# Optimization experiments

Hardware: AMD Instinct MI355X
Metric: run time of the kernel (lower is better)

## Reference

```python
import jax, jax.numpy as jnp
import numpy as np

MAX_DIST = 20
N_HEADS = 8
LN_EPS = 1e-5


def _layer_norm(x, g, b):
    mu = jnp.mean(x, axis=-1, keepdims=True)
    var = jnp.var(x, axis=-1, keepdims=True)
    return (x - mu) / jnp.sqrt(var + LN_EPS) * g + b


def setup_inputs() -> dict:
    key = jax.random.key(0)
    ks = jax.random.split(key, 12)
    B, N, D, H, F = 8, 1024, 768, N_HEADS, 1024
    w = lambda k, *sh: (jax.random.normal(k, sh, jnp.float32) * 0.02)
    return {
        "x": jax.random.normal(ks[0], (B, N, D), jnp.float32),
        "node_mask": jnp.ones((B, N), jnp.int32),
        "centers": jnp.arange(B * N, dtype=jnp.float32).reshape(B, N),
        "types": jax.random.randint(ks[1], (B, N), 0, 2, jnp.int32),
        # params (torch Linear weights stored transposed as [in, out])
        "qkv_w": w(ks[2], D, 3 * D), "qkv_b": jnp.zeros((3 * D,), jnp.float32),
        "out_w": w(ks[3], D, D), "out_b": jnp.zeros((D,), jnp.float32),
        "ff1_w": w(ks[4], D, F), "ff1_b": jnp.zeros((F,), jnp.float32),
        "ff2_w": w(ks[5], F, D), "ff2_b": jnp.zeros((D,), jnp.float32),
        "ln1_g": jnp.ones((D,), jnp.float32), "ln1_b": jnp.zeros((D,), jnp.float32),
        "ln2_g": jnp.ones((D,), jnp.float32), "ln2_b": jnp.zeros((D,), jnp.float32),
        "rel_emb": w(ks[6], 2 * MAX_DIST + 1, H),  # relative-distance bias table
        "tt": w(ks[7], H, 2, 2),                   # type-pair bias table
    }


def reference(x, node_mask, centers, types,
              qkv_w, qkv_b, out_w, out_b,
              ff1_w, ff1_b, ff2_w, ff2_b,
              ln1_g, ln1_b, ln2_g, ln2_b,
              rel_emb, tt):
    B, N, D = x.shape
    H = rel_emb.shape[1]
    Dh = D // H

    qkv = x @ qkv_w + qkv_b                       # [B,N,3D]
    q, k, v = jnp.split(qkv, 3, axis=-1)
    split = lambda t: t.reshape(B, N, H, Dh).transpose(0, 2, 1, 3)  # [B,H,N,Dh]
    q, k, v = split(q), split(k), split(v)

    scores = jnp.einsum("bhid,bhjd->bhij", q, k) / np.sqrt(Dh).astype(np.float32)

    # relative-position bias: bucket clamped distance into [0, 2*max_dist]
    dist = centers[:, :, None] - centers[:, None, :]              # [B,N,N]
    idx = jnp.round(jnp.clip(dist, -MAX_DIST, MAX_DIST) + MAX_DIST).astype(jnp.int32)
    rb = rel_emb[idx].transpose(0, 3, 1, 2)                       # [B,H,N,N]

    # type-pair bias
    ti = jnp.broadcast_to(types[:, :, None], (B, N, N))
    tj = jnp.broadcast_to(types[:, None, :], (B, N, N))
    tb = tt[:, ti, tj].transpose(1, 0, 2, 3)                      # [B,H,N,N]

    scores = scores + rb + tb
    mask = node_mask[:, None, None, :]                            # [B,1,1,N]
    scores = jnp.where(mask == 0, -jnp.inf, scores)
    att = jax.nn.softmax(scores, axis=-1)
    att = jnp.nan_to_num(att, nan=0.0)

    y = jnp.einsum("bhij,bhjd->bhid", att, v)
    y = y.transpose(0, 2, 1, 3).reshape(B, N, D)
    y = y @ out_w + out_b

    x = _layer_norm(x + y, ln1_g, ln1_b)
    ff = jax.nn.gelu(x @ ff1_w + ff1_b, approximate=False) @ ff2_w + ff2_b
    x = _layer_norm(x + ff, ln2_g, ln2_b)
    return x
```

## Files before the change

kernel.cpp:

```cpp
#include <hip/hip_runtime.h>

typedef short short8 __attribute__((ext_vector_type(8)));
typedef unsigned short ushort8v __attribute__((ext_vector_type(8)));
typedef float f32x4 __attribute__((ext_vector_type(4)));

static __device__ __forceinline__ unsigned short f2b(float f) {
    unsigned int u = __builtin_bit_cast(unsigned int, f);
    unsigned int r = (u + 0x7fffu + ((u >> 16) & 1u)) >> 16;
    return (unsigned short)r;
}
static __device__ __forceinline__ unsigned short f2b_trunc(float f) {
    return (unsigned short)(__builtin_bit_cast(unsigned int, f) >> 16);
}
static __device__ __forceinline__ float b2f(unsigned short u) {
    return __builtin_bit_cast(float, (unsigned int)u << 16);
}
static __device__ __forceinline__ float exp2v(float x) {
    float r;
    asm("v_exp_f32 %0, %1" : "=v"(r) : "v"(x));
    return r;
}

__device__ __forceinline__ void gload16(void* lds, const void* g) {
    __builtin_amdgcn_global_load_lds(
        (const __attribute__((address_space(1))) void*)g,
        (__attribute__((address_space(3))) void*)lds, 16, 0, 0);
}

#define L2E 1.4426950408889634f

__global__ __launch_bounds__(256) void prep_kernel(
    const float* __restrict__ x, unsigned short* __restrict__ xb,
    const float* __restrict__ qkv_w, unsigned short* __restrict__ qwT,
    const float* __restrict__ out_w, unsigned short* __restrict__ owT,
    const float* __restrict__ ff1_w, unsigned short* __restrict__ f1T,
    const float* __restrict__ ff2_w, unsigned short* __restrict__ f2T) {
    const int bx = blockIdx.x;
    const int tid = threadIdx.x;
    if (bx < 6144) {
        int i = bx * 256 + tid;
        float4 f = ((const float4*)x)[i];
        ushort4 u;
        u.x = f2b(f.x); u.y = f2b(f.y); u.z = f2b(f.z); u.w = f2b(f.w);
        ((ushort4*)xb)[i] = u;
        return;
    }
    __shared__ float t[32][33];
    int rb = bx - 6144;
    const float* W; unsigned short* Wt; int K, N;
    if (rb < 1728)      { W = qkv_w; Wt = qwT; K = 768;  N = 2304; }
    else if (rb < 2304) { rb -= 1728; W = out_w; Wt = owT; K = 768;  N = 768; }
    else if (rb < 3072) { rb -= 2304; W = ff1_w; Wt = f1T; K = 768;  N = 1024; }
    else                { rb -= 3072; W = ff2_w; Wt = f2T; K = 1024; N = 768; }
    const int nbl = N / 32;
    const int nb = (rb % nbl) * 32, kb = (rb / nbl) * 32;
    const int tx = tid & 31, ty = tid >> 5;
#pragma unroll
    for (int i = 0; i < 32; i += 8)
        t[ty + i][tx] = W[(size_t)(kb + ty + i) * N + nb + tx];
    __syncthreads();
#pragma unroll
    for (int i = 0; i < 32; i += 8)
        Wt[(size_t)(nb + ty + i) * K + kb + tx] = f2b(t[tx][ty + i]);
}

template <int EPI>
__global__ __launch_bounds__(512, 4) void gemm2p(
    const unsigned short* __restrict__ A, const unsigned short* __restrict__ Bt,
    const float* __restrict__ bias, float* __restrict__ outf,
    unsigned short* __restrict__ outb, unsigned short* __restrict__ q_o,
    unsigned short* __restrict__ k_o, unsigned short* __restrict__ v_o,
    int N, int K, int ntn, int NT) {
    __shared__ unsigned short a_lds[2][8192];
    __shared__ unsigned short b_lds[2][8192];
    const int tid = threadIdx.x;
    const int wave = tid >> 6, lane = tid & 63;
    const int lr = lane & 15, lg = lane >> 4;
    const int wm = wave >> 2, wn = wave & 3;
    const int nwg = gridDim.x;
    const int orig = blockIdx.x;
    const int swz = (orig & 7) * (nwg >> 3) + (orig >> 3);
    const int tm = swz / ntn, tn = swz % ntn;

    const unsigned short* srcA[2];
    const unsigned short* srcB[2];
#pragma unroll
    for (int i = 0; i < 2; ++i) {
        int g = i * 512 + tid;
        int row = g >> 3, sl = g & 7;
        int colg = sl ^ (row & 7);
        srcA[i] = A + (size_t)(tm * 128 + row) * K + colg * 8;
        srcB[i] = Bt + (size_t)(tn * 128 + row) * K + colg * 8;
    }
    auto stage = [&](int buf, int k0) {
#pragma unroll
        for (int i = 0; i < 2; ++i) {
            gload16(&a_lds[buf][i * 4096 + wave * 512], srcA[i] + k0);
            gload16(&b_lds[buf][i * 4096 + wave * 512], srcB[i] + k0);
        }
    };

    f32x4 acc[4][2] = {};

    stage(0, 0);
    asm volatile("s_waitcnt vmcnt(0)" ::: "memory");
    __builtin_amdgcn_s_barrier();

    for (int t = 0; t < NT; ++t) {
        const int buf = t & 1;
        if (t + 1 < NT) stage(buf ^ 1, (t + 1) * 64);
#pragma unroll
        for (int ks = 0; ks < 2; ++ks) {
            short8 af[4], bfr[2];
#pragma unroll
            for (int mf = 0; mf < 4; ++mf) {
                int row = wm * 64 + mf * 16 + lr;
                int slot = (ks * 4 + lg) ^ (row & 7);
                af[mf] = *(const short8*)&a_lds[buf][row * 64 + slot * 8];
            }
#pragma unroll
            for (int nf = 0; nf < 2; ++nf) {
                int row = wn * 32 + nf * 16 + lr;
                int slot = (ks * 4 + lg) ^ (row & 7);
                bfr[nf] = *(const short8*)&b_lds[buf][row * 64 + slot * 8];
            }
#pragma unroll
            for (int mf = 0; mf < 4; ++mf)
#pragma unroll
                for (int nf = 0; nf < 2; ++nf)
                    acc[mf][nf] = __builtin_amdgcn_mfma_f32_16x16x32_bf16(af[mf], bfr[nf], acc[mf][nf], 0, 0, 0);
        }
        asm volatile("s_waitcnt vmcnt(0)" ::: "memory");
        __builtin_amdgcn_s_barrier();
    }

#pragma unroll
    for (int nf = 0; nf < 2; ++nf) {
        int gc = tn * 128 + wn * 32 + nf * 16 + lr;
        float bv = bias[gc];
        int part = 0, h = 0, dh = 0;
        if constexpr (EPI == 3) {
            part = gc / 768;
            int cc = gc - part * 768;
            h = cc / 96;
            dh = cc - h * 96;
        }
#pragma unroll
        for (int mf = 0; mf < 4; ++mf) {
            int grb = tm * 128 + wm * 64 + mf * 16 + lg * 4;
            if constexpr (EPI == 3) {
                int b = grb >> 10, n2 = grb & 1023;
                size_t bh = (size_t)(b * 8 + h);
                if (part == 2) {
                    ushort4 wv;
                    wv.x = f2b(acc[mf][nf][0] + bv);
                    wv.y = f2b(acc[mf][nf][1] + bv);
                    wv.z = f2b(acc[mf][nf][2] + bv);
                    wv.w = f2b(acc[mf][nf][3] + bv);
                    *(ushort4*)&v_o[(bh * 96 + dh) * 1024 + n2] = wv;
                } else {
                    unsigned short* dst = (part == 0) ? q_o : k_o;
                    float sc = (part == 0) ? 0.14724445f : 1.f;
#pragma unroll
                    for (int r = 0; r < 4; ++r)
                        dst[(bh * 1024 + n2 + r) * 96 + dh] = f2b((acc[mf][nf][r] + bv) * sc);
                }
            } else {
#pragma unroll
                for (int r = 0; r < 4; ++r) {
                    int gr = grb + r;
                    float v = acc[mf][nf][r] + bv;
                    if constexpr (EPI == 0) {
                        outf[(size_t)gr * N + gc] = v;
                    } else if constexpr (EPI == 1) {
                        outb[(size_t)gr * N + gc] = f2b(v);
                    } else {
                        float gl = 0.5f * v * (1.f + erff(v * 0.70710678f));
                        outb[(size_t)gr * N + gc] = f2b(gl);
                    }
                }
            }
        }
    }
}

__global__ __launch_bounds__(512, 4) void attn_kernel(
    const unsigned short* __restrict__ Qb, const unsigned short* __restrict__ Kb,
    const unsigned short* __restrict__ Vt, const float* __restrict__ centers,
    const int* __restrict__ types, const int* __restrict__ nmask,
    const float* __restrict__ tt, const float* __restrict__ rel_emb,
    unsigned short* __restrict__ Y) {
    __shared__ unsigned short kv_lds[2 * 12288];
    __shared__ unsigned short p_lds[8 * 1024];
    __shared__ float c_lds[1024];
    __shared__ unsigned int bab_lds[1024];
    __shared__ float rel_lds[41];

    const int tid = threadIdx.x;
    const int wave = tid >> 6, lane = tid & 63;
    const int lr = lane & 15, lg = lane >> 4;
    const int bh = blockIdx.x, qb = blockIdx.y;
    const int b = bh >> 3, h = bh & 7;
    const int q0 = qb * 128 + wave * 16;
    const size_t kvbase = (size_t)bh * 1024 * 96;

    c_lds[tid] = centers[b * 1024 + tid];
    c_lds[tid + 512] = centers[b * 1024 + 512 + tid];
    if (tid < 41) rel_lds[tid] = rel_emb[tid * 8 + h] * L2E;
    {
        const float t00 = tt[h * 4], t01 = tt[h * 4 + 1];
        const float t10 = tt[h * 4 + 2], t11 = tt[h * 4 + 3];
#pragma unroll
        for (int i = 0; i < 2; ++i) {
            int j = tid + i * 512;
            int tj = types[b * 1024 + j];
            int mk = nmask[b * 1024 + j];
            float bA = L2E * (t00 + (t01 - t00) * tj) + (mk ? 0.f : -1e30f);
            float bB = L2E * ((t10 - t00) + (t11 - t01 - t10 + t00) * tj);
            bab_lds[j] = (unsigned)f2b(bA) | ((unsigned)f2b(bB) << 16);
        }
    }

    const unsigned short* sbase[3];
    int sstep[3];
#pragma unroll
    for (int it = 0; it < 3; ++it) {
        int g = it * 512 + tid;
        if (g < 768) {
            int ks = g >> 8, rem = g & 255, pr = rem >> 3, sl = rem & 7;
            int so = sl ^ (pr & 7);
            int r = ((so >> 2) << 5) + pr, oct = so & 3;
            sbase[it] = Kb + kvbase + (size_t)r * 96 + ks * 32 + oct * 8;
            sstep[it] = 64 * 96;
        } else {
            int gv = g - 768, pr = gv >> 3, sl = gv & 7;
            int so = sl ^ (pr & 7);
            sbase[it] = Vt + (size_t)(bh * 96 + pr) * 1024 + so * 8;
            sstep[it] = 64;
        }
    }
    auto stage = [&](int bufb, int kt) {
        unsigned short* dst = kv_lds + bufb * 12288;
#pragma unroll
        for (int it = 0; it < 3; ++it)
            gload16(dst + it * 4096 + wave * 512, sbase[it] + (size_t)kt * sstep[it]);
    };

    short8 qa[3];
#pragma unroll
    for (int ks = 0; ks < 3; ++ks)
        qa[ks] = *(const short8*)&Qb[kvbase + (size_t)(q0 + lr) * 96 + ks * 32 + lg * 8];
    short8 qa3 = {};
    {
        int ti0 = types[b * 1024 + q0 + lr];
        if (lg == 0) {
            qa3[0] = (short)0x3F80;
            qa3[1] = ti0 ? (short)0x3F80 : (short)0;
        }
    }
    float ci20[4];
#pragma unroll
    for (int r = 0; r < 4; ++r) ci20[r] = centers[b * 1024 + q0 + lg * 4 + r] + 20.f;

    float cimax20 = fmaxf(fmaxf(ci20[0], ci20[1]), fmaxf(ci20[2], ci20[3]));
    float cimin20 = fminf(fminf(ci20[0], ci20[1]), fminf(ci20[2], ci20[3]));
    cimax20 = fmaxf(cimax20, __shfl_xor(cimax20, 16));
    cimax20 = fmaxf(cimax20, __shfl_xor(cimax20, 32));
    cimin20 = fminf(cimin20, __shfl_xor(cimin20, 16));
    cimin20 = fminf(cimin20, __shfl_xor(cimin20, 32));

    short8 vone = {};
    if (lr == 0) {
#pragma unroll
        for (int e = 0; e < 8; ++e) vone[e] = (short)0x3F80;
    }

    float m_r[4] = {-3e30f, -3e30f, -3e30f, -3e30f};
    f32x4 oacc[7] = {};

    stage(0, 0);
    asm volatile("s_waitcnt lgkmcnt(0)" ::: "memory");
    const float rel0v = rel_lds[0], rel40v = rel_lds[40];

    for (int kt = 0; kt < 16; ++kt) {
        const int buf = kt & 1;
        if (kt < 15) {
            stage(buf ^ 1, kt + 1);
            asm volatile("s_waitcnt vmcnt(3)" ::: "memory");
        } else {
            asm volatile("s_waitcnt vmcnt(0)" ::: "memory");
        }
        __builtin_amdgcn_s_barrier();
        const unsigned short* kv = kv_lds + buf * 12288;

        f32x4 s[4] = {};
#pragma unroll
        for (int jf = 0; jf < 4; ++jf) {
            int pr = ((jf & 1) << 4) + lr;
            int slp = (((jf >> 1) << 2) + lg) ^ (lr & 7);
#pragma unroll
            for (int ks = 0; ks < 3; ++ks) {
                short8 kf = *(const short8*)&kv[ks * 2048 + pr * 64 + slp * 8];
                s[jf] = __builtin_amdgcn_mfma_f32_16x16x32_bf16(qa[ks], kf, s[jf], 0, 0, 0);
            }
            unsigned vb = bab_lds[kt * 64 + jf * 16 + lr];
            short8 kf3 = {};
            if (lg == 0) {
                kf3[0] = (short)(vb & 0xffffu);
                kf3[1] = (short)(vb >> 16);
            }
            s[jf] = __builtin_amdgcn_mfma_f32_16x16x32_bf16(qa3, kf3, s[jf], 0, 0, 0);
        }

        {
            float cj[4];
#pragma unroll
            for (int jf = 0; jf < 4; ++jf) cj[jf] = c_lds[kt * 64 + jf * 16 + lr];
            float cjmx = fmaxf(fmaxf(cj[0], cj[1]), fmaxf(cj[2], cj[3]));
            float cjmn = fminf(fminf(cj[0], cj[1]), fminf(cj[2], cj[3]));
#pragma unroll
            for (int off = 1; off < 16; off <<= 1) {
                cjmx = fmaxf(cjmx, __shfl_xor(cjmx, off));
                cjmn = fminf(cjmn, __shfl_xor(cjmn, off));
            }
            bool flatHi = (cimin20 - cjmx >= 40.f);
            bool flatLo = (cimax20 - cjmn <= 0.f);
            if (flatHi || flatLo) {
                float re = flatHi ? rel40v : rel0v;
#pragma unroll
                for (int jf = 0; jf < 4; ++jf)
#pragma unroll
                    for (int r = 0; r < 4; ++r) s[jf][r] += re;
            } else {
#pragma unroll
                for (int jf = 0; jf < 4; ++jf)
#pragma unroll
                    for (int r = 0; r < 4; ++r) {
                        float idxf = __builtin_amdgcn_fmed3f(ci20[r] - cj[jf], 0.f, 40.f);
                        s[jf][r] += rel_lds[(int)rintf(idxf)];
                    }
            }
        }

#pragma unroll
        for (int r = 0; r < 4; ++r) {
            float mlr = fmaxf(fmaxf(s[0][r], s[1][r]), fmaxf(s[2][r], s[3][r]));
            if (!__all(mlr <= m_r[r] + 8.f)) {
                float mx = mlr;
#pragma unroll
                for (int off = 1; off < 16; off <<= 1) mx = fmaxf(mx, __shfl_xor(mx, off));
                float mn = fmaxf(m_r[r], mx);
                float al = exp2v(m_r[r] - mn);
                m_r[r] = mn;
#pragma unroll
                for (int nf = 0; nf < 7; ++nf) oacc[nf][r] *= al;
            }
#pragma unroll
            for (int jf = 0; jf < 4; ++jf) s[jf][r] = exp2v(s[jf][r] - m_r[r]);
        }

#pragma unroll
        for (int jf = 0; jf < 4; ++jf)
#pragma unroll
            for (int r = 0; r < 4; ++r) {
                int row = lg * 4 + r, col = jf * 16 + lr;
                int gp = (col >> 3) ^ (row & 7);
                p_lds[wave * 1024 + row * 64 + gp * 8 + (col & 7)] = f2b_trunc(s[jf][r]);
            }
        asm volatile("s_waitcnt lgkmcnt(0)" ::: "memory");
        short8 pa[2];
#pragma unroll
        for (int js = 0; js < 2; ++js) {
            int slp = ((js << 2) + lg) ^ (lr & 7);
            pa[js] = *(const short8*)&p_lds[wave * 1024 + lr * 64 + slp * 8];
        }

#pragma unroll
        for (int nf = 0; nf < 6; ++nf) {
            int vrow = nf * 16 + lr;
#pragma unroll
            for (int js = 0; js < 2; ++js) {
                int slp = ((js << 2) + lg) ^ (lr & 7);
                short8 vf = *(const short8*)&kv[6144 + vrow * 64 + slp * 8];
                oacc[nf] = __builtin_amdgcn_mfma_f32_16x16x32_bf16(pa[js], vf, oacc[nf], 0, 0, 0);
            }
        }
#pragma unroll
        for (int js = 0; js < 2; ++js)
            oacc[6] = __builtin_amdgcn_mfma_f32_16x16x32_bf16(pa[js], vone, oacc[6], 0, 0, 0);
        __builtin_amdgcn_s_barrier();
    }

#pragma unroll
    for (int r = 0; r < 4; ++r) {
        float l = __shfl(oacc[6][r], lane & 48);
        float inv = (l > 0.f) ? 1.f / l : 0.f;
        int qi = q0 + lg * 4 + r;
#pragma unroll
        for (int nf = 0; nf < 6; ++nf)
            Y[((size_t)b * 1024 + qi) * 768 + h * 96 + nf * 16 + lr] = f2b(oacc[nf][r] * inv);
    }
}

template <bool IN1BF, bool IN2BF>
__global__ __launch_bounds__(384) void ln_kernel(const void* __restrict__ in1,
                                                 const void* __restrict__ in2,
                                                 const float* __restrict__ g,
                                                 const float* __restrict__ be,
                                                 float* __restrict__ of,
                                                 unsigned short* __restrict__ ob) {
    const int tid = threadIdx.x;
    const int half = tid / 192;
    const int t = tid - half * 192;
    const int row = blockIdx.x * 2 + half;
    const size_t base = (size_t)row * 768 + t * 4;
    float a[4], bb[4];
    if (IN1BF) {
        ushort4 u = *(const ushort4*)((const unsigned short*)in1 + base);
        a[0] = b2f(u.x); a[1] = b2f(u.y); a[2] = b2f(u.z); a[3] = b2f(u.w);
    } else {
        float4 u = *(const float4*)((const float*)in1 + base);
        a[0] = u.x; a[1] = u.y; a[2] = u.z; a[3] = u.w;
    }
    if (IN2BF) {
        ushort4 u = *(const ushort4*)((const unsigned short*)in2 + base);
        bb[0] = b2f(u.x); bb[1] = b2f(u.y); bb[2] = b2f(u.z); bb[3] = b2f(u.w);
    } else {
        float4 u = *(const float4*)((const float*)in2 + base);
        bb[0] = u.x; bb[1] = u.y; bb[2] = u.z; bb[3] = u.w;
    }
    float v[4];
#pragma unroll
    for (int i = 0; i < 4; ++i) v[i] = a[i] + bb[i];
    float s1 = v[0] + v[1] + v[2] + v[3];
    float s2 = v[0] * v[0] + v[1] * v[1] + v[2] * v[2] + v[3] * v[3];
#pragma unroll
    for (int off = 32; off > 0; off >>= 1) {
        s1 += __shfl_xor(s1, off);
        s2 += __shfl_xor(s2, off);
    }
    __shared__ float red[12];
    const int wv = tid >> 6;
    if ((tid & 63) == 0) { red[wv] = s1; red[6 + wv] = s2; }
    __syncthreads();
    const int w0 = half * 3;
    s1 = red[w0] + red[w0 + 1] + red[w0 + 2];
    s2 = red[6 + w0] + red[6 + w0 + 1] + red[6 + w0 + 2];
    float mu = s1 * (1.f / 768.f);
    float var = s2 * (1.f / 768.f) - mu * mu;
    float inv = rsqrtf(var + 1e-5f);
    float o[4];
#pragma unroll
    for (int i = 0; i < 4; ++i)
        o[i] = (v[i] - mu) * inv * g[t * 4 + i] + be[t * 4 + i];
    if (of) {
        float4 w = {o[0], o[1], o[2], o[3]};
        *(float4*)(of + base) = w;
    }
    if (ob) {
        ushort4 w = {f2b(o[0]), f2b(o[1]), f2b(o[2]), f2b(o[3])};
        *(ushort4*)(ob + base) = w;
    }
}

extern "C" void kernel_launch(void* const* d_in, const int* in_sizes, int n_in,
                              void* d_out, int out_size, void* d_ws, size_t ws_size,
                              hipStream_t stream) {
    const float* x     = (const float*)d_in[0];
    const int*   nmask = (const int*)d_in[1];
    const float* cent  = (const float*)d_in[2];
    const int*   types = (const int*)d_in[3];
    const float* qkv_w = (const float*)d_in[4];
    const float* qkv_b = (const float*)d_in[5];
    const float* out_w = (const float*)d_in[6];
    const float* out_b = (const float*)d_in[7];
    const float* ff1_w = (const float*)d_in[8];
    const float* ff1_b = (const float*)d_in[9];
    const float* ff2_w = (const float*)d_in[10];
    const float* ff2_b = (const float*)d_in[11];
    const float* ln1_g = (const float*)d_in[12];
    const float* ln1_b = (const float*)d_in[13];
    const float* ln2_g = (const float*)d_in[14];
    const float* ln2_b = (const float*)d_in[15];
    const float* rel   = (const float*)d_in[16];
    const float* ttp   = (const float*)d_in[17];

    char* w = (char*)d_ws;
    auto alloc = [&](size_t bytes) {
        char* p = w;
        w += (bytes + 255) & ~(size_t)255;
        return p;
    };
    unsigned short* xb  = (unsigned short*)alloc(8192ull * 768 * 2);
    unsigned short* qwT = (unsigned short*)alloc(2304ull * 768 * 2);
    unsigned short* owT = (unsigned short*)alloc(768ull * 768 * 2);
    unsigned short* f1T = (unsigned short*)alloc(1024ull * 768 * 2);
    unsigned short* f2T = (unsigned short*)alloc(768ull * 1024 * 2);
    unsigned short* Qb  = (unsigned short*)alloc(64ull * 1024 * 96 * 2);
    unsigned short* Kb  = (unsigned short*)alloc(64ull * 1024 * 96 * 2);
    unsigned short* Vt  = (unsigned short*)alloc(64ull * 96 * 1024 * 2);
    unsigned short* aob = (unsigned short*)alloc(8192ull * 768 * 2);
    unsigned short* h1b = (unsigned short*)alloc(8192ull * 768 * 2);
    unsigned short* ffa = Qb;

    prep_kernel<<<9984, 256, 0, stream>>>(x, xb, qkv_w, qwT, out_w, owT,
                                          ff1_w, f1T, ff2_w, f2T);

    gemm2p<3><<<1152, 512, 0, stream>>>(xb, qwT, qkv_b, nullptr, nullptr,
                                        Qb, Kb, Vt, 2304, 768, 18, 12);
    attn_kernel<<<dim3(64, 8), 512, 0, stream>>>(Qb, Kb, Vt, cent, types, nmask, ttp, rel, xb);
    gemm2p<1><<<384, 512, 0, stream>>>(xb, owT, out_b, nullptr, aob,
                                       nullptr, nullptr, nullptr, 768, 768, 6, 12);
    ln_kernel<false, true><<<4096, 384, 0, stream>>>(x, aob, ln1_g, ln1_b, nullptr, h1b);
    gemm2p<2><<<512, 512, 0, stream>>>(h1b, f1T, ff1_b, nullptr, ffa,
                                       nullptr, nullptr, nullptr, 1024, 768, 8, 12);
    gemm2p<1><<<384, 512, 0, stream>>>(ffa, f2T, ff2_b, nullptr, aob,
                                       nullptr, nullptr, nullptr, 768, 1024, 6, 16);
    ln_kernel<true, true><<<4096, 384, 0, stream>>>(h1b, aob, ln2_g, ln2_b, (float*)d_out, nullptr);
}
```

Measured before the change: 197.1 us.

## Transpose QK^T MFMA output so softmax rows live per lane

Swaps the MFMA operand order so each lane holds one query row's scores across columns. The softmax max and sum then need only cross-lane-group shuffles, the row sum is accumulated in registers instead of through an extra ones-vector MFMA, and P is written to LDS as packed bf16 pairs with v_cvt_pk_bf16. The rescale factor now has to be shuffled back into the output-accumulator layout, and the P-to-LDS write uses a new swizzle that must match the read pattern. P also changes from truncated to rounded bf16 conversion.

```diff
diff --git a/kernel.cpp b/kernel.cpp
--- a/kernel.cpp
+++ b/kernel.cpp
@@ -9,15 +9,17 @@
     unsigned int r = (u + 0x7fffu + ((u >> 16) & 1u)) >> 16;
     return (unsigned short)r;
 }
-static __device__ __forceinline__ unsigned short f2b_trunc(float f) {
-    return (unsigned short)(__builtin_bit_cast(unsigned int, f) >> 16);
-}
 static __device__ __forceinline__ float b2f(unsigned short u) {
     return __builtin_bit_cast(float, (unsigned int)u << 16);
 }
 static __device__ __forceinline__ float exp2v(float x) {
     float r;
     asm("v_exp_f32 %0, %1" : "=v"(r) : "v"(x));
+    return r;
+}
+static __device__ __forceinline__ unsigned cvt_pk_bf16(float lo, float hi) {
+    unsigned r;
+    asm("v_cvt_pk_bf16_f32 %0, %1, %2" : "=v"(r) : "v"(lo), "v"(hi));
     return r;
 }
 
@@ -258,25 +260,17 @@
             qa3[1] = ti0 ? (short)0x3F80 : (short)0;
         }
     }
-    float ci20[4];
-#pragma unroll
-    for (int r = 0; r < 4; ++r) ci20[r] = centers[b * 1024 + q0 + lg * 4 + r] + 20.f;
-
-    float cimax20 = fmaxf(fmaxf(ci20[0], ci20[1]), fmaxf(ci20[2], ci20[3]));
-    float cimin20 = fminf(fminf(ci20[0], ci20[1]), fminf(ci20[2], ci20[3]));
-    cimax20 = fmaxf(cimax20, __shfl_xor(cimax20, 16));
-    cimax20 = fmaxf(cimax20, __shfl_xor(cimax20, 32));
-    cimin20 = fminf(cimin20, __shfl_xor(cimin20, 16));
-    cimin20 = fminf(cimin20, __shfl_xor(cimin20, 32));
-
-    short8 vone = {};
-    if (lr == 0) {
-#pragma unroll
-        for (int e = 0; e < 8; ++e) vone[e] = (short)0x3F80;
-    }
-
-    float m_r[4] = {-3e30f, -3e30f, -3e30f, -3e30f};
-    f32x4 oacc[7] = {};
+    const float ci20 = centers[b * 1024 + q0 + lr] + 20.f;
+    float cimax20 = ci20, cimin20 = ci20;
+#pragma unroll
+    for (int off = 1; off < 16; off <<= 1) {
+        cimax20 = fmaxf(cimax20, __shfl_xor(cimax20, off));
+        cimin20 = fminf(cimin20, __shfl_xor(cimin20, off));
+    }
+
+    float m_s = -3e30f, l_s = 0.f;
+    f32x4 oacc[6] = {};
+    unsigned* p32 = (unsigned*)&p_lds[wave * 1024];
 
     stage(0, 0);
     asm volatile("s_waitcnt lgkmcnt(0)" ::: "memory");
@@ -301,7 +295,7 @@
 #pragma unroll
             for (int ks = 0; ks < 3; ++ks) {
                 short8 kf = *(const short8*)&kv[ks * 2048 + pr * 64 + slp * 8];
-                s[jf] = __builtin_amdgcn_mfma_f32_16x16x32_bf16(qa[ks], kf, s[jf], 0, 0, 0);
+                s[jf] = __builtin_amdgcn_mfma_f32_16x16x32_bf16(kf, qa[ks], s[jf], 0, 0, 0);
             }
             unsigned vb = bab_lds[kt * 64 + jf * 16 + lr];
             short8 kf3 = {};
@@ -309,20 +303,24 @@
                 kf3[0] = (short)(vb & 0xffffu);
                 kf3[1] = (short)(vb >> 16);
             }
-            s[jf] = __builtin_amdgcn_mfma_f32_16x16x32_bf16(qa3, kf3, s[jf], 0, 0, 0);
+            s[jf] = __builtin_amdgcn_mfma_f32_16x16x32_bf16(kf3, qa3, s[jf], 0, 0, 0);
         }
 
         {
-            float cj[4];
-#pragma unroll
-            for (int jf = 0; jf < 4; ++jf) cj[jf] = c_lds[kt * 64 + jf * 16 + lr];
-            float cjmx = fmaxf(fmaxf(cj[0], cj[1]), fmaxf(cj[2], cj[3]));
-            float cjmn = fminf(fminf(cj[0], cj[1]), fminf(cj[2], cj[3]));
-#pragma unroll
-            for (int off = 1; off < 16; off <<= 1) {
-                cjmx = fmaxf(cjmx, __shfl_xor(cjmx, off));
-                cjmn = fminf(cjmn, __shfl_xor(cjmn, off));
-            }
+            float4 cj4[4];
+#pragma unroll
+            for (int jf = 0; jf < 4; ++jf)
+                cj4[jf] = *(const float4*)&c_lds[kt * 64 + jf * 16 + lg * 4];
+            float cjmx = cj4[0].x, cjmn = cj4[0].x;
+#pragma unroll
+            for (int jf = 0; jf < 4; ++jf) {
+                cjmx = fmaxf(cjmx, fmaxf(fmaxf(cj4[jf].x, cj4[jf].y), fmaxf(cj4[jf].z, cj4[jf].w)));
+                cjmn = fminf(cjmn, fminf(fminf(cj4[jf].x, cj4[jf].y), fminf(cj4[jf].z, cj4[jf].w)));
+            }
+            cjmx = fmaxf(cjmx, __shfl_xor(cjmx, 16));
+            cjmx = fmaxf(cjmx, __shfl_xor(cjmx, 32));
+            cjmn = fminf(cjmn, __shfl_xor(cjmn, 16));
+            cjmn = fminf(cjmn, __shfl_xor(cjmn, 32));
             bool flatHi = (cimin20 - cjmx >= 40.f);
             bool flatLo = (cimax20 - cjmn <= 0.f);
             if (flatHi || flatLo) {
@@ -332,47 +330,67 @@
 #pragma unroll
                     for (int r = 0; r < 4; ++r) s[jf][r] += re;
             } else {
+                float cjl[4][4] = {{cj4[0].x, cj4[0].y, cj4[0].z, cj4[0].w},
+                                   {cj4[1].x, cj4[1].y, cj4[1].z, cj4[1].w},
+                                   {cj4[2].x, cj4[2].y, cj4[2].z, cj4[2].w},
+                                   {cj4[3].x, cj4[3].y, cj4[3].z, cj4[3].w}};
 #pragma unroll
                 for (int jf = 0; jf < 4; ++jf)
 #pragma unroll
                     for (int r = 0; r < 4; ++r) {
-                        float idxf = __builtin_amdgcn_fmed3f(ci20[r] - cj[jf], 0.f, 40.f);
+                        float idxf = __builtin_amdgcn_fmed3f(ci20 - cjl[jf][r], 0.f, 40.f);
                         s[jf][r] += rel_lds[(int)rintf(idxf)];
                     }
             }
         }
 
-#pragma unroll
-        for (int r = 0; r < 4; ++r) {
-            float mlr = fmaxf(fmaxf(s[0][r], s[1][r]), fmaxf(s[2][r], s[3][r]));
-            if (!__all(mlr <= m_r[r] + 8.f)) {
-                float mx = mlr;
-#pragma unroll
-                for (int off = 1; off < 16; off <<= 1) mx = fmaxf(mx, __shfl_xor(mx, off));
-                float mn = fmaxf(m_r[r], mx);
-                float al = exp2v(m_r[r] - mn);
-                m_r[r] = mn;
-#pragma unroll
-                for (int nf = 0; nf < 7; ++nf) oacc[nf][r] *= al;
-            }
-#pragma unroll
-            for (int jf = 0; jf < 4; ++jf) s[jf][r] = exp2v(s[jf][r] - m_r[r]);
-        }
-
-#pragma unroll
-        for (int jf = 0; jf < 4; ++jf)
-#pragma unroll
-            for (int r = 0; r < 4; ++r) {
-                int row = lg * 4 + r, col = jf * 16 + lr;
-                int gp = (col >> 3) ^ (row & 7);
-                p_lds[wave * 1024 + row * 64 + gp * 8 + (col & 7)] = f2b_trunc(s[jf][r]);
-            }
+        {
+            float mlr = s[0][0];
+#pragma unroll
+            for (int jf = 0; jf < 4; ++jf)
+#pragma unroll
+                for (int r = 0; r < 4; ++r) mlr = fmaxf(mlr, s[jf][r]);
+            if (!__all(mlr <= m_s + 8.f)) {
+                float mx = fmaxf(mlr, __shfl_xor(mlr, 16));
+                mx = fmaxf(mx, __shfl_xor(mx, 32));
+                float mn = fmaxf(m_s, mx);
+                float al = exp2v(m_s - mn);
+                m_s = mn;
+                l_s *= al;
+#pragma unroll
+                for (int r = 0; r < 4; ++r) {
+                    float alr = __shfl(al, lg * 4 + r);
+#pragma unroll
+                    for (int nf = 0; nf < 6; ++nf) oacc[nf][r] *= alr;
+                }
+            }
+            float ls = 0.f;
+#pragma unroll
+            for (int jf = 0; jf < 4; ++jf)
+#pragma unroll
+                for (int r = 0; r < 4; ++r) {
+                    s[jf][r] = exp2v(s[jf][r] - m_s);
+                    ls += s[jf][r];
+                }
+            ls += __shfl_xor(ls, 16);
+            ls += __shfl_xor(ls, 32);
+            l_s += ls;
+        }
+
+#pragma unroll
+        for (int jf = 0; jf < 4; ++jf) {
+            uint2 w2;
+            w2.x = cvt_pk_bf16(s[jf][0], s[jf][1]);
+            w2.y = cvt_pk_bf16(s[jf][2], s[jf][3]);
+            int gsw = ((jf * 4 + lg) ^ (lr & 14)) * 2;
+            *(uint2*)&p32[lr * 32 + gsw] = w2;
+        }
         asm volatile("s_waitcnt lgkmcnt(0)" ::: "memory");
         short8 pa[2];
 #pragma unroll
         for (int js = 0; js < 2; ++js) {
-            int slp = ((js << 2) + lg) ^ (lr & 7);
-            pa[js] = *(const short8*)&p_lds[wave * 1024 + lr * 64 + slp * 8];
+            int gsw = (((js * 8 + lg * 2) ^ (lr & 14))) * 2;
+            pa[js] = *(const short8*)&p32[lr * 32 + gsw];
         }
 
 #pragma unroll
@@ -385,16 +403,13 @@
                 oacc[nf] = __builtin_amdgcn_mfma_f32_16x16x32_bf16(pa[js], vf, oacc[nf], 0, 0, 0);
             }
         }
-#pragma unroll
-        for (int js = 0; js < 2; ++js)
-            oacc[6] = __builtin_amdgcn_mfma_f32_16x16x32_bf16(pa[js], vone, oacc[6], 0, 0, 0);
         __builtin_amdgcn_s_barrier();
     }
 
 #pragma unroll
     for (int r = 0; r < 4; ++r) {
-        float l = __shfl(oacc[6][r], lane & 48);
-        float inv = (l > 0.f) ? 1.f / l : 0.f;
+        float lrow = __shfl(l_s, lg * 4 + r);
+        float inv = (lrow > 0.f) ? 1.f / lrow : 0.f;
         int qi = q0 + lg * 4 + r;
 #pragma unroll
         for (int nf = 0; nf < 6; ++nf)
```

Measured after the change: 186.5 us. 1.06x faster.
